# Kernel optimization log

Measured on AMD Instinct MI355X. Metric: run time of the kernel, lower is better.

The kernel has to match this reference:

```python
import jax, jax.numpy as jnp
import numpy as np

MIN_BIN_W = 1e-3
MIN_BIN_H = 1e-3
MIN_DERIV = 1e-3
EPS = 1e-6


def _mlp(x, W0, b0, W1, b1, W2, b2):
    h = jax.nn.relu(x @ W0 + b0)
    h = jax.nn.relu(h @ W1 + b1)
    return h @ W2 + b2


def _rqs_forward(inputs, widths, heights, derivatives):
    # inputs: [B, D]; widths/heights: [B, D, nb]; derivatives: [B, D, nb-1]
    nb = widths.shape[-1]
    inputs = jnp.clip(inputs, 0.0, 1.0)
    widths = jax.nn.softmax(widths, axis=-1)
    heights = jax.nn.softmax(heights, axis=-1)
    widths = MIN_BIN_W + (1.0 - MIN_BIN_W * nb) * widths
    heights = MIN_BIN_H + (1.0 - MIN_BIN_H * nb) * heights
    derivatives = jax.nn.softplus(derivatives) + MIN_DERIV

    pad2 = [(0, 0), (0, 0)]
    x_knots = jnp.pad(jnp.cumsum(widths, axis=-1), pad2 + [(1, 0)])   # [B,D,nb+1]
    y_knots = jnp.pad(jnp.cumsum(heights, axis=-1), pad2 + [(1, 0)])
    derivs = jnp.pad(derivatives, pad2 + [(1, 1)], constant_values=1.0)  # [B,D,nb+1]

    # searchsorted (side='left'): count of knots strictly less than input
    bin_idx = jnp.sum(x_knots < inputs[..., None], axis=-1)
    bin_idx = jnp.clip(bin_idx, 1, nb)[..., None]  # [B,D,1]

    g = lambda a, i: jnp.take_along_axis(a, i, axis=-1)[..., 0]
    x_k = g(x_knots, bin_idx - 1)
    y_k = g(y_knots, bin_idx - 1)
    w_k = g(widths, bin_idx - 1)
    h_k = g(heights, bin_idx - 1)
    d_k = g(derivs, bin_idx - 1)
    d_k1 = g(derivs, bin_idx)

    s_k = h_k / w_k
    theta = (inputs - x_k) / w_k
    t1t = theta * (1.0 - theta)
    den = s_k + (d_k + d_k1 - 2.0 * s_k) * t1t
    outputs = y_k + h_k * (s_k * theta ** 2 + d_k * t1t) / (den + EPS)
    nom_d = s_k ** 2 * (d_k1 * theta ** 2 + 2.0 * s_k * t1t + d_k * (1.0 - theta) ** 2)
    log_det = jnp.log(nom_d / (den ** 2 + EPS))
    return outputs, log_det


def setup_inputs() -> dict:
    key = jax.random.key(0)
    ks = jax.random.split(key, 7)
    B, D, H, NB = 65536, 64, 512, 8
    out_dim = D * (3 * NB - 1)
    inp = {
        "x": jax.random.uniform(ks[0], (B, D), dtype=jnp.float32),
        "W0": jax.random.normal(ks[1], (D, H), dtype=jnp.float32) * 0.05,
        "b0": jnp.zeros((H,), jnp.float32),
        "W1": jax.random.normal(ks[2], (H, H), dtype=jnp.float32) * 0.05,
        "b1": jnp.zeros((H,), jnp.float32),
        "W2": jax.random.normal(ks[3], (H, out_dim), dtype=jnp.float32) * 0.05,
        "b2": jnp.zeros((out_dim,), jnp.float32),
        "num_bins": NB,
    }
    return inp


def reference(x, W0, b0, W1, b1, W2, b2, num_bins):
    B, D = x.shape
    nb = int(num_bins)
    params = _mlp(x, W0, b0, W1, b1, W2, b2).reshape(B, D, 3 * nb - 1)
    widths = params[..., :nb]
    heights = params[..., nb:2 * nb]
    derivatives = params[..., 2 * nb:]
    z, log_det = _rqs_forward(x, widths, heights, derivatives)
    return z, jnp.sum(log_det, axis=1)
```

## Files before the change

kernel.cpp:

```cpp
#include <hip/hip_runtime.h>

typedef unsigned short u16;
typedef __bf16 bf16x8 __attribute__((ext_vector_type(8)));
typedef float f32x4 __attribute__((ext_vector_type(4)));

__device__ __forceinline__ u16 f2bf_r(float f) {
    union { float f; unsigned u; } v; v.f = f;
    return (u16)((v.u + 0x8000u) >> 16);
}
__device__ __forceinline__ float rcpf(float x) { return __builtin_amdgcn_rcpf(x); }

__device__ __forceinline__ void gload_lds16(const u16* g, u16* l) {
    __builtin_amdgcn_global_load_lds(
        (const __attribute__((address_space(1))) void*)g,
        (__attribute__((address_space(3))) void*)l,
        16, 0, 0);
}


#define BM 128
#define BN 128
#define BK 32

template<int K, int RELU, int NBX>
__global__ __launch_bounds__(256) void gemm_bt(
    const u16* __restrict__ A, const u16* __restrict__ BT,
    const float* __restrict__ bias, u16* __restrict__ C,
    int M, int N)
{
    constexpr int NS = K / BK;
    __shared__ u16 smem[3 * 8192];
    const int t = threadIdx.x;
    const int lane = t & 63;
    const int wave = t >> 6;
    const int wr = (wave >> 1) * 64;
    const int wc = (wave & 1) * 64;

    const int nlin = blockIdx.x;
    const int jj = nlin >> 3;
    const long brow = (long)((nlin & 7) + 8 * (jj / NBX)) * BM;
    const long bcol = (long)(jj % NBX) * BN;

    const int sr = t >> 2;
    const int sc = ((t & 3) ^ ((t >> 3) & 3)) * 8;
    const u16* gA0 = A + (brow + sr) * (long)K + sc;
    const u16* gA1 = gA0 + 64L * K;
    const u16* gB0 = BT + (bcol + sr) * (long)K + sc;
    const u16* gB1 = gB0 + 64L * K;

    f32x4 acc[4][4] = {};
    const int fr = lane & 15;
    const int fbase = fr * 32 + (((lane >> 4) ^ ((fr >> 1) & 3)) * 8);

    auto STAGE = [&](int buf, int k0) {
        u16* As = &smem[buf * 8192];
        u16* Bs = As + 4096;
        gload_lds16(gA0 + k0, &As[t * 8]);
        gload_lds16(gA1 + k0, &As[2048 + t * 8]);
        gload_lds16(gB0 + k0, &Bs[t * 8]);
        gload_lds16(gB1 + k0, &Bs[2048 + t * 8]);
    };
    auto COMPUTE = [&](int buf) {
        const u16* As = &smem[buf * 8192];
        const u16* Bs = As + 4096;
        bf16x8 af[4], bfr[4];
#pragma unroll
        for (int m = 0; m < 4; ++m)
            af[m] = *(const bf16x8*)&As[wr * 32 + m * 512 + fbase];
#pragma unroll
        for (int n = 0; n < 4; ++n)
            bfr[n] = *(const bf16x8*)&Bs[wc * 32 + n * 512 + fbase];
#pragma unroll
        for (int m = 0; m < 4; ++m)
#pragma unroll
            for (int n = 0; n < 4; ++n)
                acc[m][n] = __builtin_amdgcn_mfma_f32_16x16x32_bf16(
                    af[m], bfr[n], acc[m][n], 0, 0, 0);
    };

    STAGE(0, 0);
    STAGE(1, BK);
#pragma unroll
    for (int i = 0; i < NS; ++i) {
        if (i < NS - 1) asm volatile("s_waitcnt vmcnt(4)" ::: "memory");
        else            asm volatile("s_waitcnt vmcnt(0)" ::: "memory");
        __builtin_amdgcn_s_barrier();
        __builtin_amdgcn_sched_barrier(0);
        if (i + 2 < NS) STAGE((i + 2) % 3, (i + 2) * BK);
        COMPUTE(i % 3);
    }

#pragma unroll
    for (int n = 0; n < 4; ++n) {
        const long col = bcol + wc + n * 16 + fr;
        const float bv = bias[col];
#pragma unroll
        for (int m = 0; m < 4; ++m) {
            const long row = brow + wr + m * 16 + (lane >> 4) * 4;
#pragma unroll
            for (int j = 0; j < 4; ++j) {
                float v = acc[m][n][j] + bv;
                if (RELU) v = fmaxf(v, 0.f);
                C[(row + j) * (long)N + col] = f2bf_r(v);
            }
        }
    }
}

#define G3_BM 256
#define G3_BN 192
#define G3_BK 64
#define G3_BUF 28672
#define G3_BOFF 16384
#define CLS 200

template<int K>
__global__ __launch_bounds__(512, 2) void gemm3_rqs(
    const u16* __restrict__ A,
    const u16* __restrict__ BT,
    const float* __restrict__ bias,
    const float* __restrict__ x,
    float* __restrict__ z,
    float* __restrict__ ldp)
{
    constexpr int NT = K / G3_BK;
    __shared__ u16 smem[2 * G3_BUF];

    const int t = threadIdx.x;
    const int lane = t & 63;
    const int wave = t >> 6;
    const int wm = wave >> 2;
    const int wn = wave & 3;

    const int nlin = blockIdx.x;
    const int bx = (nlin >> 3) & 7;
    const long BROW = ((long)(nlin & 7) + 8 * (nlin >> 6)) * G3_BM;
    const int bcol = bx * G3_BN;

    const int rowp = (t & 255) >> 2;
    const int kcol = (((t & 3) ^ ((t >> 3) & 3)) * 8) + ((t & 256) ? 32 : 0);
    const u16* gA = A + (BROW + rowp) * (long)K + kcol;
    const u16* gB = BT + ((long)bcol + rowp) * K + kcol;

    f32x4 acc[8][3] = {};
    const int fr = lane & 15;
    const int gsel = ((lane >> 4) ^ ((fr >> 1) & 3)) * 8;

    int a_off[8];
#pragma unroll
    for (int m = 0; m < 8; ++m) {
        int ra = wm * 128 + m * 16 + fr;
        a_off[m] = (ra >> 6) * 4096 + (ra & 63) * 32 + gsel;
    }
    int b_off[3];
#pragma unroll
    for (int nn = 0; nn < 3; ++nn) {
        int rb = wn * 48 + nn * 16 + fr;
        b_off[nn] = G3_BOFF + (rb >> 6) * 4096 + (rb & 63) * 32 + gsel;
    }

    auto STAGE = [&](int tile, int buf) {
        const long ko = (long)tile * G3_BK;
        u16* dst = &smem[buf * G3_BUF];
#pragma unroll
        for (int r = 0; r < 4; ++r)
            gload_lds16(gA + ko + (long)r * 64 * K, &dst[r * 4096 + t * 8]);
#pragma unroll
        for (int r = 0; r < 3; ++r)
            gload_lds16(gB + ko + (long)r * 64 * K, &dst[G3_BOFF + r * 4096 + t * 8]);
    };

    bf16x8 bfr[3][2], afA[2][2], afB[2][2];
    auto READ_A = [&](bf16x8 (&af)[2][2], int q, const u16* Ab) {
#pragma unroll
        for (int md = 0; md < 2; ++md)
#pragma unroll
            for (int h = 0; h < 2; ++h)
                af[md][h] = *(const bf16x8*)&Ab[a_off[q * 2 + md] + h * 2048];
    };
    auto MFMA_Q = [&](bf16x8 (&af)[2][2], int q) {
#pragma unroll
        for (int md = 0; md < 2; ++md)
#pragma unroll
            for (int nn = 0; nn < 3; ++nn)
#pragma unroll
                for (int h = 0; h < 2; ++h)
                    acc[q * 2 + md][nn] = __builtin_amdgcn_mfma_f32_16x16x32_bf16(
                        af[md][h], bfr[nn][h], acc[q * 2 + md][nn], 0, 0, 0);
    };

    STAGE(0, 0);
    STAGE(1, 1);
    asm volatile("s_waitcnt vmcnt(7)" ::: "memory");
    __builtin_amdgcn_s_barrier();
    __builtin_amdgcn_sched_barrier(0);

#pragma unroll
    for (int i = 0; i < NT; ++i) {
        const int cur = i & 1;
        const u16* Ab = &smem[cur * G3_BUF];

#pragma unroll
        for (int nn = 0; nn < 3; ++nn)
#pragma unroll
            for (int h = 0; h < 2; ++h)
                bfr[nn][h] = *(const bf16x8*)&Ab[b_off[nn] + h * 2048];
        READ_A(afA, 0, Ab);
        READ_A(afB, 1, Ab);
        __builtin_amdgcn_s_setprio(1); MFMA_Q(afA, 0); __builtin_amdgcn_s_setprio(0);
        __builtin_amdgcn_s_barrier();
        __builtin_amdgcn_sched_barrier(0);

        READ_A(afA, 2, Ab);
        __builtin_amdgcn_s_setprio(1); MFMA_Q(afB, 1); __builtin_amdgcn_s_setprio(0);
        __builtin_amdgcn_s_barrier();
        __builtin_amdgcn_sched_barrier(0);

        READ_A(afB, 3, Ab);
        __builtin_amdgcn_s_setprio(1); MFMA_Q(afA, 2); __builtin_amdgcn_s_setprio(0);
        asm volatile("s_waitcnt lgkmcnt(0)" ::: "memory");
        __builtin_amdgcn_sched_barrier(0);
        __builtin_amdgcn_s_barrier();
        __builtin_amdgcn_sched_barrier(0);

        if (i + 2 < NT) STAGE(i + 2, cur);
        __builtin_amdgcn_s_setprio(1); MFMA_Q(afB, 3); __builtin_amdgcn_s_setprio(0);
        if (i < NT - 2) asm volatile("s_waitcnt vmcnt(7)" ::: "memory");
        else            asm volatile("s_waitcnt vmcnt(0)" ::: "memory");
        __builtin_amdgcn_s_barrier();
        __builtin_amdgcn_sched_barrier(0);
    }

    __syncthreads();

#pragma unroll
    for (int nn = 0; nn < 3; ++nn) {
        const int cl = wn * 48 + nn * 16 + fr;
        const float bv = bias[bcol + cl];
#pragma unroll
        for (int m = 0; m < 8; ++m) {
            const int rl = wm * 128 + m * 16 + (lane >> 4) * 4;
#pragma unroll
            for (int j = 0; j < 4; ++j)
                smem[(rl + j) * CLS + cl] = f2bf_r(acc[m][nn][j] + bv);
        }
    }
    __syncthreads();

    const int dbase = bx * 8;
#pragma unroll
    for (int pi = 0; pi < 4; ++pi) {
        const int p  = t + pi * 512;
        const int bl = p >> 3;
        const int dl = p & 7;
        const u16* pp = &smem[bl * CLS + dl * 24];
        bf16x8 v0 = *(const bf16x8*)(pp);
        bf16x8 v1 = *(const bf16x8*)(pp + 8);
        bf16x8 v2 = *(const bf16x8*)(pp + 16);

        float w[8], h[8];
        float sw = 0.f, sh = 0.f;
#pragma unroll
        for (int i = 0; i < 8; ++i) { w[i] = __expf((float)v0[i]); sw += w[i]; }
#pragma unroll
        for (int i = 0; i < 8; ++i) { h[i] = __expf((float)v1[i]); sh += h[i]; }
        const float rw = 0.992f * rcpf(sw);
        const float rh = 0.992f * rcpf(sh);
#pragma unroll
        for (int i = 0; i < 8; ++i) w[i] = fmaf(w[i], rw, 0.001f);
#pragma unroll
        for (int i = 0; i < 8; ++i) h[i] = fmaf(h[i], rh, 0.001f);

        const long b = BROW + bl;
        const int  d = dbase + dl;
        float xin = x[b * 64 + d];
        xin = fminf(fmaxf(xin, 0.f), 1.f);

        float x_k = 0.f, y_k = 0.f, w_k = w[0], h_k = h[0];
        float rk = 0.f, rk1 = (float)v2[0];
        bool isfirst = true, islast = false;
        float cw = 0.f, ch = 0.f;
#pragma unroll
        for (int i = 1; i < 8; ++i) {
            cw += w[i - 1]; ch += h[i - 1];
            if (cw < xin) {
                x_k = cw; y_k = ch; w_k = w[i]; h_k = h[i];
                rk = (float)v2[i - 1];
                rk1 = (i < 7) ? (float)v2[i] : 0.f;
                isfirst = false; islast = (i == 7);
            }
        }
        float sp_k  = __logf(1.f + __expf(rk));
        float sp_k1 = __logf(1.f + __expf(rk1));
        float d_k  = isfirst ? 1.f : sp_k  + 0.001f;
        float d_k1 = islast  ? 1.f : sp_k1 + 0.001f;

        const float inv_wk = rcpf(w_k);
        const float s   = h_k * inv_wk;
        const float th  = (xin - x_k) * inv_wk;
        const float omt = 1.f - th;
        const float t1t = th * omt;
        const float den = fmaf(d_k + d_k1 - 2.f * s, t1t, s);
        const float num = fmaf(s * th, th, d_k * t1t);
        const float out = fmaf(h_k * num, rcpf(den + 1e-6f), y_k);
        const float nom = s * s * fmaf(d_k1 * th, th, fmaf(2.f * s, t1t, d_k * omt * omt));
        const float logdet = __logf(nom) - __logf(fmaf(den, den, 1e-6f));

        z[b * 64 + d]   = out;
        ldp[b * 64 + d] = logdet;
    }
}

__global__ __launch_bounds__(256) void ld_reduce(
    const float* __restrict__ ldp, float* __restrict__ ld)
{
    const int b = blockIdx.x * 4 + (threadIdx.x >> 6);
    const int lane = threadIdx.x & 63;
    float r = ldp[(long)b * 64 + lane];
#pragma unroll
    for (int off = 32; off; off >>= 1) r += __shfl_xor(r, off, 64);
    if (lane == 0) ld[b] = r;
}

__global__ void cvt_x_bf16(const float* __restrict__ in, u16* __restrict__ out, long n) {
    long i = (long)blockIdx.x * blockDim.x + threadIdx.x;
    long stride = (long)gridDim.x * blockDim.x;
    for (; i < n; i += stride) out[i] = f2bf_r(in[i]);
}

__global__ void transpose_w_bf16(const float* __restrict__ W, u16* __restrict__ WT,
                                 int K, int N) {
    long total = (long)N * K;
    long i = (long)blockIdx.x * blockDim.x + threadIdx.x;
    long stride = (long)gridDim.x * blockDim.x;
    for (; i < total; i += stride) {
        int n = (int)(i / K), k = (int)(i % K);
        WT[i] = f2bf_r(W[(long)k * N + n]);
    }
}

__global__ void transpose_w2_bf16(const float* __restrict__ W, u16* __restrict__ WT, int K) {
    long total = 1536L * K;
    long i = (long)blockIdx.x * blockDim.x + threadIdx.x;
    long stride = (long)gridDim.x * blockDim.x;
    for (; i < total; i += stride) {
        int npad = (int)(i / K), k = (int)(i % K);
        int g = npad / 24, r = npad % 24;
        float v = (r < 23) ? W[(long)k * 1472 + g * 23 + r] : 0.f;
        WT[i] = f2bf_r(v);
    }
}

__global__ void pad_bias2(const float* __restrict__ b2, float* __restrict__ b2p) {
    int c = blockIdx.x * 256 + threadIdx.x;
    if (c < 1536) {
        int g = c / 24, r = c % 24;
        b2p[c] = (r < 23) ? b2[g * 23 + r] : 0.f;
    }
}

__global__ void fill_fail(float* __restrict__ out, long n) {
    long i = (long)blockIdx.x * blockDim.x + threadIdx.x;
    long stride = (long)gridDim.x * blockDim.x;
    for (; i < n; i += stride) out[i] = -1.0f;
}

extern "C" void kernel_launch(void* const* d_in, const int* in_sizes, int n_in,
                              void* d_out, int out_size, void* d_ws, size_t ws_size,
                              hipStream_t stream)
{
    const float* x  = (const float*)d_in[0];
    const float* W0 = (const float*)d_in[1];
    const float* b0 = (const float*)d_in[2];
    const float* W1 = (const float*)d_in[3];
    const float* b1 = (const float*)d_in[4];
    const float* W2 = (const float*)d_in[5];
    const float* b2 = (const float*)d_in[6];
    const int B = in_sizes[0] / 64;
    const int D = 64, H = 512, NP = 1536;

    char* ws = (char*)d_ws;
    size_t off = 0;
    u16* W0T = (u16*)(ws + off); off += (size_t)H * D * 2;
    u16* W1T = (u16*)(ws + off); off += (size_t)H * H * 2;
    u16* W2T = (u16*)(ws + off); off += (size_t)NP * H * 2;
    float* b2p = (float*)(ws + off); off += (size_t)NP * 4;
    off = (off + 255) & ~(size_t)255;
    u16*   h1  = (u16*)(ws + off);
    float* ldp = (float*)(ws + off);
    off += (size_t)B * H * 2;
    u16* xb = (u16*)(ws + off);
    u16* h2 = (u16*)(ws + off);
    off += (size_t)B * H * 2;
    size_t need = off;

    float* zout  = (float*)d_out;
    float* ldout = zout + (size_t)B * D;

    if (ws_size < need) {
        fill_fail<<<2048, 256, 0, stream>>>(zout, (long)out_size);
        return;
    }

    cvt_x_bf16<<<2048, 256, 0, stream>>>(x, xb, (long)B * D);
    transpose_w_bf16<<<128, 256, 0, stream>>>(W0, W0T, D, H);
    transpose_w_bf16<<<1024, 256, 0, stream>>>(W1, W1T, H, H);
    transpose_w2_bf16<<<3072, 256, 0, stream>>>(W2, W2T, H);
    pad_bias2<<<6, 256, 0, stream>>>(b2, b2p);

    gemm_bt<64, 1, 4><<<2048, 256, 0, stream>>>(xb, W0T, b0, h1, B, H);
    gemm_bt<512, 1, 4><<<2048, 256, 0, stream>>>(h1, W1T, b1, h2, B, H);

    gemm3_rqs<512><<<2048, 512, 0, stream>>>(h2, W2T, b2p, x, zout, ldp);

    ld_reduce<<<B / 4, 256, 0, stream>>>(ldp, ldout);
}
```

Baseline: 232.8 us.

## Rearrange gemm3 wave layout to 4x2 with 64x96 per-wave tiles

Changes the per-wave tile in the fused third GEMM and RQS kernel from 128x48 (waves laid out 2x4) to 64x96 (waves laid out 4x2). Each wave now loads 4 A fragments and 6 B fragments per K-step instead of 8 and 3, which lowers LDS read traffic per MFMA. The four-phase MFMA/barrier pipeline is rebuilt as quadrant passes that reuse the A and B fragment registers between phases, and the epilogue indexing is updated to match. Register pressure and the interleaving of LDS reads with MFMAs both change under launch_bounds(512,2).

```diff
diff --git a/kernel.cpp b/kernel.cpp
--- a/kernel.cpp
+++ b/kernel.cpp
@@ -129,8 +129,8 @@
     const int t = threadIdx.x;
     const int lane = t & 63;
     const int wave = t >> 6;
-    const int wm = wave >> 2;
-    const int wn = wave & 3;
+    const int wm = wave >> 1;
+    const int wn = wave & 1;
 
     const int nlin = blockIdx.x;
     const int bx = (nlin >> 3) & 7;
@@ -142,20 +142,20 @@
     const u16* gA = A + (BROW + rowp) * (long)K + kcol;
     const u16* gB = BT + ((long)bcol + rowp) * K + kcol;
 
-    f32x4 acc[8][3] = {};
+    f32x4 acc[4][6] = {};
     const int fr = lane & 15;
     const int gsel = ((lane >> 4) ^ ((fr >> 1) & 3)) * 8;
 
-    int a_off[8];
-#pragma unroll
-    for (int m = 0; m < 8; ++m) {
-        int ra = wm * 128 + m * 16 + fr;
+    int a_off[4];
+#pragma unroll
+    for (int m = 0; m < 4; ++m) {
+        int ra = wm * 64 + m * 16 + fr;
         a_off[m] = (ra >> 6) * 4096 + (ra & 63) * 32 + gsel;
     }
-    int b_off[3];
-#pragma unroll
-    for (int nn = 0; nn < 3; ++nn) {
-        int rb = wn * 48 + nn * 16 + fr;
+    int b_off[6];
+#pragma unroll
+    for (int nn = 0; nn < 6; ++nn) {
+        int rb = wn * 96 + nn * 16 + fr;
         b_off[nn] = G3_BOFF + (rb >> 6) * 4096 + (rb & 63) * 32 + gsel;
     }
 
@@ -170,24 +170,7 @@
             gload_lds16(gB + ko + (long)r * 64 * K, &dst[G3_BOFF + r * 4096 + t * 8]);
     };
 
-    bf16x8 bfr[3][2], afA[2][2], afB[2][2];
-    auto READ_A = [&](bf16x8 (&af)[2][2], int q, const u16* Ab) {
-#pragma unroll
-        for (int md = 0; md < 2; ++md)
-#pragma unroll
-            for (int h = 0; h < 2; ++h)
-                af[md][h] = *(const bf16x8*)&Ab[a_off[q * 2 + md] + h * 2048];
-    };
-    auto MFMA_Q = [&](bf16x8 (&af)[2][2], int q) {
-#pragma unroll
-        for (int md = 0; md < 2; ++md)
-#pragma unroll
-            for (int nn = 0; nn < 3; ++nn)
-#pragma unroll
-                for (int h = 0; h < 2; ++h)
-                    acc[q * 2 + md][nn] = __builtin_amdgcn_mfma_f32_16x16x32_bf16(
-                        af[md][h], bfr[nn][h], acc[q * 2 + md][nn], 0, 0, 0);
-    };
+    bf16x8 aF[4][2], bF0[3][2], bF1[3][2];
 
     STAGE(0, 0);
     STAGE(1, 1);
@@ -201,30 +184,77 @@
         const u16* Ab = &smem[cur * G3_BUF];
 
 #pragma unroll
+        for (int m = 0; m < 2; ++m)
+#pragma unroll
+            for (int h = 0; h < 2; ++h)
+                aF[m][h] = *(const bf16x8*)&Ab[a_off[m] + h * 2048];
+#pragma unroll
         for (int nn = 0; nn < 3; ++nn)
 #pragma unroll
             for (int h = 0; h < 2; ++h)
-                bfr[nn][h] = *(const bf16x8*)&Ab[b_off[nn] + h * 2048];
-        READ_A(afA, 0, Ab);
-        READ_A(afB, 1, Ab);
-        __builtin_amdgcn_s_setprio(1); MFMA_Q(afA, 0); __builtin_amdgcn_s_setprio(0);
+                bF0[nn][h] = *(const bf16x8*)&Ab[b_off[nn] + h * 2048];
+        __builtin_amdgcn_s_setprio(1);
+#pragma unroll
+        for (int m = 0; m < 2; ++m)
+#pragma unroll
+            for (int nn = 0; nn < 3; ++nn)
+#pragma unroll
+                for (int h = 0; h < 2; ++h)
+                    acc[m][nn] = __builtin_amdgcn_mfma_f32_16x16x32_bf16(
+                        aF[m][h], bF0[nn][h], acc[m][nn], 0, 0, 0);
+        __builtin_amdgcn_s_setprio(0);
         __builtin_amdgcn_s_barrier();
         __builtin_amdgcn_sched_barrier(0);
 
-        READ_A(afA, 2, Ab);
-        __builtin_amdgcn_s_setprio(1); MFMA_Q(afB, 1); __builtin_amdgcn_s_setprio(0);
+#pragma unroll
+        for (int nn = 0; nn < 3; ++nn)
+#pragma unroll
+            for (int h = 0; h < 2; ++h)
+                bF1[nn][h] = *(const bf16x8*)&Ab[b_off[3 + nn] + h * 2048];
+        __builtin_amdgcn_s_setprio(1);
+#pragma unroll
+        for (int m = 0; m < 2; ++m)
+#pragma unroll
+            for (int nn = 0; nn < 3; ++nn)
+#pragma unroll
+                for (int h = 0; h < 2; ++h)
+                    acc[m][3 + nn] = __builtin_amdgcn_mfma_f32_16x16x32_bf16(
+                        aF[m][h], bF1[nn][h], acc[m][3 + nn], 0, 0, 0);
+        __builtin_amdgcn_s_setprio(0);
         __builtin_amdgcn_s_barrier();
         __builtin_amdgcn_sched_barrier(0);
 
-        READ_A(afB, 3, Ab);
-        __builtin_amdgcn_s_setprio(1); MFMA_Q(afA, 2); __builtin_amdgcn_s_setprio(0);
+#pragma unroll
+        for (int m = 0; m < 2; ++m)
+#pragma unroll
+            for (int h = 0; h < 2; ++h)
+                aF[2 + m][h] = *(const bf16x8*)&Ab[a_off[2 + m] + h * 2048];
+        __builtin_amdgcn_s_setprio(1);
+#pragma unroll
+        for (int m = 0; m < 2; ++m)
+#pragma unroll
+            for (int nn = 0; nn < 3; ++nn)
+#pragma unroll
+                for (int h = 0; h < 2; ++h)
+                    acc[2 + m][3 + nn] = __builtin_amdgcn_mfma_f32_16x16x32_bf16(
+                        aF[2 + m][h], bF1[nn][h], acc[2 + m][3 + nn], 0, 0, 0);
+        __builtin_amdgcn_s_setprio(0);
         asm volatile("s_waitcnt lgkmcnt(0)" ::: "memory");
         __builtin_amdgcn_sched_barrier(0);
         __builtin_amdgcn_s_barrier();
         __builtin_amdgcn_sched_barrier(0);
 
         if (i + 2 < NT) STAGE(i + 2, cur);
-        __builtin_amdgcn_s_setprio(1); MFMA_Q(afB, 3); __builtin_amdgcn_s_setprio(0);
+        __builtin_amdgcn_s_setprio(1);
+#pragma unroll
+        for (int m = 0; m < 2; ++m)
+#pragma unroll
+            for (int nn = 0; nn < 3; ++nn)
+#pragma unroll
+                for (int h = 0; h < 2; ++h)
+                    acc[2 + m][nn] = __builtin_amdgcn_mfma_f32_16x16x32_bf16(
+                        aF[2 + m][h], bF0[nn][h], acc[2 + m][nn], 0, 0, 0);
+        __builtin_amdgcn_s_setprio(0);
         if (i < NT - 2) asm volatile("s_waitcnt vmcnt(7)" ::: "memory");
         else            asm volatile("s_waitcnt vmcnt(0)" ::: "memory");
         __builtin_amdgcn_s_barrier();
@@ -234,12 +264,12 @@
     __syncthreads();
 
 #pragma unroll
-    for (int nn = 0; nn < 3; ++nn) {
-        const int cl = wn * 48 + nn * 16 + fr;
+    for (int nn = 0; nn < 6; ++nn) {
+        const int cl = wn * 96 + nn * 16 + fr;
         const float bv = bias[bcol + cl];
 #pragma unroll
-        for (int m = 0; m < 8; ++m) {
-            const int rl = wm * 128 + m * 16 + (lane >> 4) * 4;
+        for (int m = 0; m < 4; ++m) {
+            const int rl = wm * 64 + m * 16 + (lane >> 4) * 4;
 #pragma unroll
             for (int j = 0; j < 4; ++j)
                 smem[(rl + j) * CLS + cl] = f2bf_r(acc[m][nn][j] + bv);
```

Result: no change. 232.6 us (-0.1%).
